# Kernel optimization log

Measured on AMD Instinct MI355X. Metric: run time of the kernel, lower is better.

Reference implementation:

```python
import jax, jax.numpy as jnp
import numpy as np

EPS = 1e-5

def layer_norm(x, g, b):
    m = x.mean(-1, keepdims=True)
    v = ((x - m) ** 2).mean(-1, keepdims=True)
    return (x - m) * jax.lax.rsqrt(v + EPS) * g + b

def setup_inputs() -> dict:
    key = jax.random.key(0)
    ks = jax.random.split(key, 8)
    H, T = 512, 256
    hidden_states = jax.random.normal(ks[0], (1, T, H), jnp.float32)
    U = jax.random.normal(ks[1], (H, H), jnp.float32) * 0.01
    W = jax.random.normal(ks[2], (H, H), jnp.float32) * 0.01
    a = jax.random.normal(ks[3], (H,), jnp.float32) * 0.01
    b = jax.random.normal(ks[4], (H,), jnp.float32) * 0.01
    gamma = jnp.ones((H,), jnp.float32)
    beta = jnp.zeros((H,), jnp.float32)
    targets = jax.random.randint(ks[5], (T,), 0, H)  # deterministic stand-in for torch.randint dummy targets
    return {"hidden_states": hidden_states, "U": U, "W": W, "a": a, "b": b,
            "gamma": gamma, "beta": beta, "targets": targets}

def reference(hidden_states, U, W, a, b, gamma, beta, targets):
    # batch must be 1 (torch.outer in the original requires 1-D vectors)
    h = hidden_states[0]                      # (T, H)
    z = jax.nn.relu(h @ U + a)                # (T, H) slow-path hidden

    # Per-timestep grads of CE(LayerNorm(z_t @ W + b), target_t) w.r.t. W, b
    def step_loss(z_t, tgt, W_, b_):
        y = layer_norm(z_t @ W_ + b_, gamma, beta)
        return -jax.nn.log_softmax(y)[tgt]
    grad_fn = jax.grad(step_loss, argnums=(2, 3))
    gradW, gradb = jax.vmap(grad_fn, in_axes=(0, 0, None, None))(z, targets, W, b)  # (T,H,H), (T,H)

    # W_update_t[p,q] = sum_{i<t} h_i[p] * h_t[q] * gradW_i[p,q]
    G = h[:, :, None] * gradW                 # (T, H, H)
    A = jnp.cumsum(G, axis=0) - G             # exclusive prefix sum over i
    W_upd = A * h[:, None, :]                 # (T, H, H)
    fastW = W - jnp.cumsum(W_upd, axis=0)     # cumulative fast weights per t

    # b_update_t[q] = h_t[q] * sum_{i<t} (sum_p h_i[p]) * gradb_i[q]
    c = h.sum(-1)                             # (T,)
    Bc = c[:, None] * gradb                   # (T, H)
    Bex = jnp.cumsum(Bc, axis=0) - Bc         # exclusive
    b_upd = h * Bex
    fastb = b - jnp.cumsum(b_upd, axis=0)     # (T, H)

    pre = jnp.einsum('th,thq->tq', z, fastW) + fastb
    out = layer_norm(pre, gamma, beta)        # (T, H)
    return out[None]                          # (1, T, H)
```

## Files before the change

### kernel.cpp

```cpp
#include <hip/hip_runtime.h>

#define T 256
#define H 512
#define EPSF 1e-5f

__device__ __forceinline__ float block_sum(float v, float* s4) {
    for (int o = 32; o; o >>= 1) v += __shfl_xor(v, o);
    int w = threadIdx.x >> 6;
    __syncthreads();
    if ((threadIdx.x & 63) == 0) s4[w] = v;
    __syncthreads();
    return s4[0] + s4[1] + s4[2] + s4[3];
}

__device__ __forceinline__ float block_max(float v, float* s4) {
    for (int o = 32; o; o >>= 1) v = fmaxf(v, __shfl_xor(v, o));
    int w = threadIdx.x >> 6;
    __syncthreads();
    if ((threadIdx.x & 63) == 0) s4[w] = v;
    __syncthreads();
    return fmaxf(fmaxf(s4[0], s4[1]), fmaxf(s4[2], s4[3]));
}

__global__ __launch_bounds__(256) void k1(
        const float* __restrict__ h, const float* __restrict__ U,
        const float* __restrict__ a, float* __restrict__ Z,
        float* __restrict__ HZ, float* __restrict__ c, float* __restrict__ S) {
    int bid = blockIdx.x, tid = threadIdx.x;
    int lane = tid & 63, w = tid >> 6;
    if (bid < 8) {
        __shared__ float csum[4][64];
        int q = bid * 64 + lane;
        int tbase = w * 64;
        float s = 0.f;
        for (int j = 0; j < 64; j += 8) {
            float v[8];
            #pragma unroll
            for (int u = 0; u < 8; ++u) v[u] = h[(tbase + j + u) * H + q];
            #pragma unroll
            for (int u = 0; u < 8; ++u) s += v[u];
        }
        csum[w][lane] = s;
        __syncthreads();
        float acc = 0.f;
        #pragma unroll
        for (int w2 = 0; w2 < 3; ++w2) if (w2 < w) acc += csum[w2][lane];
        for (int j = 0; j < 64; j += 8) {
            float v[8];
            #pragma unroll
            for (int u = 0; u < 8; ++u) v[u] = h[(tbase + j + u) * H + q];
            #pragma unroll
            for (int u = 0; u < 8; ++u) { acc += v[u]; S[(tbase + j + u) * H + q] = acc; }
        }
        return;
    }
    int b = bid - 8;
    int t0 = (b >> 2) * 2, qt = b & 3;
    __shared__ __align__(16) float sh[1024];
    __shared__ float2 part[3][2][64];
    __shared__ float s4[4];
    (void)s4;
    ((float4*)sh)[tid] = ((const float4*)(h + t0 * H))[tid];
    __syncthreads();

    if (qt == 0 && w < 2) {
        float s = 0.f;
        #pragma unroll
        for (int j = 0; j < 8; ++j) s += sh[w * 512 + lane + j * 64];
        for (int o = 32; o; o >>= 1) s += __shfl_xor(s, o);
        if (lane == 0) c[t0 + w] = s;
    }

    int qc = qt * 64 + lane;
    const float2* U2 = (const float2*)U;
    float2 acc0 = {0.f, 0.f}, acc1 = {0.f, 0.f};
    int kbeg = w * 128;
    for (int k0 = kbeg; k0 < kbeg + 128; k0 += 8) {
        float2 bv[8];
        #pragma unroll
        for (int u = 0; u < 8; ++u) bv[u] = U2[(k0 + u) * 256 + qc];
        float a0[8], a1[8];
        #pragma unroll
        for (int u = 0; u < 8; ++u) { a0[u] = sh[k0 + u]; a1[u] = sh[512 + k0 + u]; }
        #pragma unroll
        for (int u = 0; u < 8; ++u) {
            acc0.x += a0[u] * bv[u].x; acc0.y += a0[u] * bv[u].y;
            acc1.x += a1[u] * bv[u].x; acc1.y += a1[u] * bv[u].y;
        }
    }
    if (w) { part[w - 1][0][lane] = acc0; part[w - 1][1][lane] = acc1; }
    __syncthreads();
    if (w == 0) {
        #pragma unroll
        for (int p = 0; p < 3; ++p) {
            acc0.x += part[p][0][lane].x; acc0.y += part[p][0][lane].y;
            acc1.x += part[p][1][lane].x; acc1.y += part[p][1][lane].y;
        }
        float2 av = ((const float2*)a)[qc];
        float z0x = fmaxf(acc0.x + av.x, 0.f), z0y = fmaxf(acc0.y + av.y, 0.f);
        float z1x = fmaxf(acc1.x + av.x, 0.f), z1y = fmaxf(acc1.y + av.y, 0.f);
        float2 h0 = ((float2*)sh)[qc], h1 = ((float2*)sh)[256 + qc];
        ((float2*)Z)[t0 * 256 + qc]        = make_float2(z0x, z0y);
        ((float2*)Z)[(t0 + 1) * 256 + qc]  = make_float2(z1x, z1y);
        ((float2*)HZ)[t0 * 256 + qc]       = make_float2(h0.x * z0x, h0.y * z0y);
        ((float2*)HZ)[(t0 + 1) * 256 + qc] = make_float2(h1.x * z1x, h1.y * z1y);
    }
}

__global__ __launch_bounds__(256) void k2(
        const float* __restrict__ Z, const float* __restrict__ W,
        const float* __restrict__ bb, const float* __restrict__ HZ,
        const float* __restrict__ c, float* __restrict__ u0,
        float* __restrict__ Beta) {
    __shared__ __align__(16) float smem[2 * 8 * 516 + 256];
    int bid = blockIdx.x, tid = threadIdx.x;
    int lane = tid & 63, w = tid >> 6;
    if (bid < 512) {
        float* sh = smem;
        float2* part = (float2*)(smem + 1024);
        int t0 = (bid >> 2) * 2, qt = bid & 3;
        ((float4*)sh)[tid] = ((const float4*)(Z + t0 * H))[tid];
        __syncthreads();
        int qc = qt * 64 + lane;
        const float2* W2 = (const float2*)W;
        float2 acc0 = {0.f, 0.f}, acc1 = {0.f, 0.f};
        int kbeg = w * 128;
        for (int k0 = kbeg; k0 < kbeg + 128; k0 += 8) {
            float2 bv[8];
            #pragma unroll
            for (int u = 0; u < 8; ++u) bv[u] = W2[(k0 + u) * 256 + qc];
            float a0[8], a1[8];
            #pragma unroll
            for (int u = 0; u < 8; ++u) { a0[u] = sh[k0 + u]; a1[u] = sh[512 + k0 + u]; }
            #pragma unroll
            for (int u = 0; u < 8; ++u) {
                acc0.x += a0[u] * bv[u].x; acc0.y += a0[u] * bv[u].y;
                acc1.x += a1[u] * bv[u].x; acc1.y += a1[u] * bv[u].y;
            }
        }
        if (w) { part[((w - 1) * 2 + 0) * 64 + lane] = acc0; part[((w - 1) * 2 + 1) * 64 + lane] = acc1; }
        __syncthreads();
        if (w == 0) {
            #pragma unroll
            for (int p = 0; p < 3; ++p) {
                float2 p0 = part[(p * 2 + 0) * 64 + lane];
                float2 p1 = part[(p * 2 + 1) * 64 + lane];
                acc0.x += p0.x; acc0.y += p0.y;
                acc1.x += p1.x; acc1.y += p1.y;
            }
            float2 bv = ((const float2*)bb)[qc];
            ((float2*)u0)[t0 * 256 + qc]       = make_float2(acc0.x + bv.x, acc0.y + bv.y);
            ((float2*)u0)[(t0 + 1) * 256 + qc] = make_float2(acc1.x + bv.x, acc1.y + bv.y);
        }
    } else {
        int b = bid - 512;
        int ti = b >> 5, ii = b & 31;
        if (ii > ti) return;
        int t0 = ti * 8, i0 = ii * 8;
        float* Zs = smem;
        float* Hs = smem + 8 * 516;
        float* red = smem + 2 * 8 * 516;
        #pragma unroll
        for (int j = 0; j < 4; ++j) {
            int idx = tid + j * 256;
            int row = idx >> 7, col4 = idx & 127;
            float4 v = ((const float4*)(Z + (t0 + row) * H))[col4];
            *(float4*)&Zs[row * 516 + col4 * 4] = v;
            float4 g = ((const float4*)(HZ + (i0 + row) * H))[col4];
            *(float4*)&Hs[row * 516 + col4 * 4] = g;
        }
        __syncthreads();
        int ks = tid >> 6, r = (tid >> 3) & 7, ci = tid & 7;
        float acc = 0.f;
        int kb = ks * 128;
        #pragma unroll 4
        for (int k0 = kb; k0 < kb + 128; k0 += 8) {
            float4 z0 = *(float4*)&Zs[r * 516 + k0];
            float4 z1 = *(float4*)&Zs[r * 516 + k0 + 4];
            float4 h0 = *(float4*)&Hs[ci * 516 + k0];
            float4 h1 = *(float4*)&Hs[ci * 516 + k0 + 4];
            acc += z0.x * h0.x + z0.y * h0.y + z0.z * h0.z + z0.w * h0.w
                 + z1.x * h1.x + z1.y * h1.y + z1.z * h1.z + z1.w * h1.w;
        }
        red[ks * 64 + r * 8 + ci] = acc;
        __syncthreads();
        if (tid < 64) {
            int r2 = tid >> 3, c2 = tid & 7;
            float v = red[tid] + red[64 + tid] + red[128 + tid] + red[192 + tid];
            int t = t0 + r2, i = i0 + c2;
            Beta[t * 256 + i] = (i < t) ? v + c[i] : 0.f;
        }
    }
}

__global__ __launch_bounds__(256) void k3(
        const float* __restrict__ u0, const float* __restrict__ gamma,
        const float* __restrict__ beta, const int* __restrict__ targets,
        const float* __restrict__ S, float* __restrict__ D, float* __restrict__ SD) {
    __shared__ float s4[4];
    int t = blockIdx.x, tid = threadIdx.x;
    float2 uv = ((const float2*)u0)[t * 256 + tid];
    float2 gv = ((const float2*)gamma)[tid];
    float2 bv = ((const float2*)beta)[tid];

    float m = block_sum(uv.x + uv.y, s4) * (1.f / H);
    float d0 = uv.x - m, d1 = uv.y - m;
    float var = block_sum(d0 * d0 + d1 * d1, s4) * (1.f / H);
    float s = rsqrtf(var + EPSF);
    float xh0 = d0 * s, xh1 = d1 * s;
    float y0 = xh0 * gv.x + bv.x;
    float y1 = xh1 * gv.y + bv.y;

    float ymax = block_max(fmaxf(y0, y1), s4);
    float e0 = __expf(y0 - ymax), e1 = __expf(y1 - ymax);
    float Zs = block_sum(e0 + e1, s4);
    float invZ = 1.f / Zs;
    int tgt = targets[t];
    float g0 = e0 * invZ - (2 * tid == tgt ? 1.f : 0.f);
    float g1 = e1 * invZ - (2 * tid + 1 == tgt ? 1.f : 0.f);
    float gy0 = g0 * gv.x, gy1 = g1 * gv.y;

    float mgy = block_sum(gy0 + gy1, s4) * (1.f / H);
    float mgx = block_sum(gy0 * xh0 + gy1 * xh1, s4) * (1.f / H);

    float dd0 = s * (gy0 - mgy - xh0 * mgx);
    float dd1 = s * (gy1 - mgy - xh1 * mgx);
    float2 sv = ((const float2*)S)[t * 256 + tid];
    ((float2*)D)[t * 256 + tid]  = make_float2(dd0, dd1);
    ((float2*)SD)[t * 256 + tid] = make_float2(sv.x * dd0, sv.y * dd1);
}

__global__ __launch_bounds__(256) void k5(
        const float* __restrict__ Beta, const float* __restrict__ D,
        const float* __restrict__ SD, float* __restrict__ A1p,
        float* __restrict__ A2p) {
    int bid = blockIdx.x, tid = threadIdx.x;
    int t = bid >> 1, kh = bid & 1;
    int qc = tid;
    int ibeg = kh * 128;
    int kup;
    if (kh == 0) kup = (t >= 128) ? 128 : ((t + 7) & ~7);
    else         kup = (t > 128) ? ((t + 7) & ~7) : 128;
    const float2* D2 = (const float2*)D;
    const float2* SD2 = (const float2*)SD;
    float2 a1 = {0.f, 0.f}, a2 = {0.f, 0.f};
    for (int k0 = ibeg; k0 < kup; k0 += 8) {
        float2 dv[8], sv[8];
        #pragma unroll
        for (int u = 0; u < 8; ++u) {
            dv[u] = D2[(k0 + u) * 256 + qc];
            sv[u] = SD2[(k0 + u) * 256 + qc];
        }
        #pragma unroll
        for (int u = 0; u < 8; ++u) {
            float bw = Beta[t * 256 + k0 + u];
            a1.x += bw * dv[u].x; a1.y += bw * dv[u].y;
            a2.x += bw * sv[u].x; a2.y += bw * sv[u].y;
        }
    }
    ((float2*)A1p)[(kh * T + t) * 256 + qc] = a1;
    ((float2*)A2p)[(kh * T + t) * 256 + qc] = a2;
}

__global__ __launch_bounds__(256) void k6(
        const float* __restrict__ A1p, const float* __restrict__ A2p,
        const float* __restrict__ u0, const float* __restrict__ S,
        const float* __restrict__ gamma, const float* __restrict__ beta,
        float* __restrict__ out) {
    __shared__ float s4[4];
    int t = blockIdx.x, tid = threadIdx.x, qc = tid;
    float2 a1a = ((const float2*)A1p)[t * 256 + qc];
    float2 a1b = ((const float2*)A1p)[(T + t) * 256 + qc];
    float2 a2a = ((const float2*)A2p)[t * 256 + qc];
    float2 a2b = ((const float2*)A2p)[(T + t) * 256 + qc];
    float2 uv = ((const float2*)u0)[t * 256 + qc];
    float2 st = ((const float2*)S)[t * 256 + qc];
    float p0 = uv.x - st.x * (a1a.x + a1b.x) + (a2a.x + a2b.x);
    float p1 = uv.y - st.y * (a1a.y + a1b.y) + (a2a.y + a2b.y);
    float m = block_sum(p0 + p1, s4) * (1.f / H);
    float d0 = p0 - m, d1 = p1 - m;
    float var = block_sum(d0 * d0 + d1 * d1, s4) * (1.f / H);
    float s = rsqrtf(var + EPSF);
    float2 gv = ((const float2*)gamma)[qc];
    float2 bv = ((const float2*)beta)[qc];
    ((float2*)out)[t * 256 + qc] = make_float2(
        d0 * s * gv.x + bv.x, d1 * s * gv.y + bv.y);
}

extern "C" void kernel_launch(void* const* d_in, const int* in_sizes, int n_in,
                              void* d_out, int out_size, void* d_ws, size_t ws_size,
                              hipStream_t stream) {
    const float* h     = (const float*)d_in[0];
    const float* U     = (const float*)d_in[1];
    const float* W     = (const float*)d_in[2];
    const float* a     = (const float*)d_in[3];
    const float* b     = (const float*)d_in[4];
    const float* gamma = (const float*)d_in[5];
    const float* beta  = (const float*)d_in[6];
    const int*   tgt   = (const int*)d_in[7];
    float* out = (float*)d_out;

    float* ws = (float*)d_ws;
    float* Z    = ws;
    float* HZ   = Z    + T * H;
    float* u0   = HZ   + T * H;
    float* D    = u0   + T * H;
    float* SD   = D    + T * H;
    float* S    = SD   + T * H;
    float* A1p  = S    + T * H;
    float* A2p  = A1p  + 2 * T * H;
    float* c    = A2p  + 2 * T * H;
    float* Beta = c    + T;

    k1<<<520,  256, 0, stream>>>(h, U, a, Z, HZ, c, S);
    k2<<<1536, 256, 0, stream>>>(Z, W, b, HZ, c, u0, Beta);
    k3<<<T,    256, 0, stream>>>(u0, gamma, beta, tgt, S, D, SD);
    k5<<<2 * T, 256, 0, stream>>>(Beta, D, SD, A1p, A2p);
    k6<<<T,    256, 0, stream>>>(A1p, A2p, u0, S, gamma, beta, out);
}
```

Baseline: 114.4 us.

## Widen GEMM row tiles, compact triangular grid, fuse prefix-sum and final LayerNorm kernels

The k1 and k2 GEMM blocks now each process 8 timesteps instead of 2. This reuses every U/W load across 8 rows and cuts the block count. The triangular Beta part of k2 now launches only the lower-triangle tiles, using a sqrt-based index decode, instead of launching a full grid and returning early. k5 and k6 are merged into one kernel that handles 4 timesteps per block and does the full k-range reduction plus the final LayerNorm, which removes the A1p/A2p intermediate buffers and one launch. The trade-off is far fewer blocks (136, 64), so the GPU may be underused, plus more register pressure.

```diff
diff --git a/kernel.cpp b/kernel.cpp
--- a/kernel.cpp
+++ b/kernel.cpp
@@ -55,55 +55,65 @@
         return;
     }
     int b = bid - 8;
-    int t0 = (b >> 2) * 2, qt = b & 3;
-    __shared__ __align__(16) float sh[1024];
-    __shared__ float2 part[3][2][64];
-    __shared__ float s4[4];
-    (void)s4;
-    ((float4*)sh)[tid] = ((const float4*)(h + t0 * H))[tid];
-    __syncthreads();
-
-    if (qt == 0 && w < 2) {
-        float s = 0.f;
-        #pragma unroll
-        for (int j = 0; j < 8; ++j) s += sh[w * 512 + lane + j * 64];
-        for (int o = 32; o; o >>= 1) s += __shfl_xor(s, o);
-        if (lane == 0) c[t0 + w] = s;
+    int t0 = (b >> 2) * 8, qt = b & 3;
+    __shared__ __align__(16) float sh[8 * 512];
+    __shared__ float2 part[3][8][64];
+    #pragma unroll
+    for (int j = 0; j < 4; ++j)
+        ((float4*)sh)[tid + j * 256] = ((const float4*)(h + t0 * H))[tid + j * 256];
+    __syncthreads();
+
+    if (qt == 0) {
+        #pragma unroll
+        for (int rr = 0; rr < 2; ++rr) {
+            int r = w * 2 + rr;
+            float s = 0.f;
+            #pragma unroll
+            for (int j = 0; j < 8; ++j) s += sh[r * 512 + lane + j * 64];
+            for (int o = 32; o; o >>= 1) s += __shfl_xor(s, o);
+            if (lane == 0) c[t0 + r] = s;
+        }
     }
 
     int qc = qt * 64 + lane;
     const float2* U2 = (const float2*)U;
-    float2 acc0 = {0.f, 0.f}, acc1 = {0.f, 0.f};
+    float2 acc[8];
+    #pragma unroll
+    for (int r = 0; r < 8; ++r) acc[r] = make_float2(0.f, 0.f);
     int kbeg = w * 128;
     for (int k0 = kbeg; k0 < kbeg + 128; k0 += 8) {
         float2 bv[8];
         #pragma unroll
         for (int u = 0; u < 8; ++u) bv[u] = U2[(k0 + u) * 256 + qc];
-        float a0[8], a1[8];
-        #pragma unroll
-        for (int u = 0; u < 8; ++u) { a0[u] = sh[k0 + u]; a1[u] = sh[512 + k0 + u]; }
-        #pragma unroll
-        for (int u = 0; u < 8; ++u) {
-            acc0.x += a0[u] * bv[u].x; acc0.y += a0[u] * bv[u].y;
-            acc1.x += a1[u] * bv[u].x; acc1.y += a1[u] * bv[u].y;
-        }
-    }
-    if (w) { part[w - 1][0][lane] = acc0; part[w - 1][1][lane] = acc1; }
+        #pragma unroll
+        for (int r = 0; r < 8; ++r) {
+            float4 f0 = *(const float4*)&sh[r * 512 + k0];
+            float4 f1 = *(const float4*)&sh[r * 512 + k0 + 4];
+            float av[8] = {f0.x, f0.y, f0.z, f0.w, f1.x, f1.y, f1.z, f1.w};
+            #pragma unroll
+            for (int u = 0; u < 8; ++u) {
+                acc[r].x += av[u] * bv[u].x;
+                acc[r].y += av[u] * bv[u].y;
+            }
+        }
+    }
+    if (w) {
+        #pragma unroll
+        for (int r = 0; r < 8; ++r) part[w - 1][r][lane] = acc[r];
+    }
     __syncthreads();
     if (w == 0) {
-        #pragma unroll
-        for (int p = 0; p < 3; ++p) {
-            acc0.x += part[p][0][lane].x; acc0.y += part[p][0][lane].y;
-            acc1.x += part[p][1][lane].x; acc1.y += part[p][1][lane].y;
-        }
-        float2 av = ((const float2*)a)[qc];
-        float z0x = fmaxf(acc0.x + av.x, 0.f), z0y = fmaxf(acc0.y + av.y, 0.f);
-        float z1x = fmaxf(acc1.x + av.x, 0.f), z1y = fmaxf(acc1.y + av.y, 0.f);
-        float2 h0 = ((float2*)sh)[qc], h1 = ((float2*)sh)[256 + qc];
-        ((float2*)Z)[t0 * 256 + qc]        = make_float2(z0x, z0y);
-        ((float2*)Z)[(t0 + 1) * 256 + qc]  = make_float2(z1x, z1y);
-        ((float2*)HZ)[t0 * 256 + qc]       = make_float2(h0.x * z0x, h0.y * z0y);
-        ((float2*)HZ)[(t0 + 1) * 256 + qc] = make_float2(h1.x * z1x, h1.y * z1y);
+        float2 av2 = ((const float2*)a)[qc];
+        #pragma unroll
+        for (int r = 0; r < 8; ++r) {
+            float2 s0 = acc[r];
+            #pragma unroll
+            for (int p = 0; p < 3; ++p) { s0.x += part[p][r][lane].x; s0.y += part[p][r][lane].y; }
+            float zx = fmaxf(s0.x + av2.x, 0.f), zy = fmaxf(s0.y + av2.y, 0.f);
+            float hx = sh[r * 512 + 2 * qc], hy = sh[r * 512 + 2 * qc + 1];
+            ((float2*)Z)[(t0 + r) * 256 + qc]  = make_float2(zx, zy);
+            ((float2*)HZ)[(t0 + r) * 256 + qc] = make_float2(hx * zx, hy * zy);
+        }
     }
 }
 
@@ -112,50 +122,63 @@
         const float* __restrict__ bb, const float* __restrict__ HZ,
         const float* __restrict__ c, float* __restrict__ u0,
         float* __restrict__ Beta) {
-    __shared__ __align__(16) float smem[2 * 8 * 516 + 256];
+    __shared__ __align__(16) float smem[8512];
     int bid = blockIdx.x, tid = threadIdx.x;
     int lane = tid & 63, w = tid >> 6;
-    if (bid < 512) {
+    if (bid < 128) {
         float* sh = smem;
-        float2* part = (float2*)(smem + 1024);
-        int t0 = (bid >> 2) * 2, qt = bid & 3;
-        ((float4*)sh)[tid] = ((const float4*)(Z + t0 * H))[tid];
+        float2* part = (float2*)(smem + 4096);
+        int t0 = (bid >> 2) * 8, qt = bid & 3;
+        #pragma unroll
+        for (int j = 0; j < 4; ++j)
+            ((float4*)sh)[tid + j * 256] = ((const float4*)(Z + t0 * H))[tid + j * 256];
         __syncthreads();
         int qc = qt * 64 + lane;
         const float2* W2 = (const float2*)W;
-        float2 acc0 = {0.f, 0.f}, acc1 = {0.f, 0.f};
+        float2 acc[8];
+        #pragma unroll
+        for (int r = 0; r < 8; ++r) acc[r] = make_float2(0.f, 0.f);
         int kbeg = w * 128;
         for (int k0 = kbeg; k0 < kbeg + 128; k0 += 8) {
             float2 bv[8];
             #pragma unroll
             for (int u = 0; u < 8; ++u) bv[u] = W2[(k0 + u) * 256 + qc];
-            float a0[8], a1[8];
-            #pragma unroll
-            for (int u = 0; u < 8; ++u) { a0[u] = sh[k0 + u]; a1[u] = sh[512 + k0 + u]; }
-            #pragma unroll
-            for (int u = 0; u < 8; ++u) {
-                acc0.x += a0[u] * bv[u].x; acc0.y += a0[u] * bv[u].y;
-                acc1.x += a1[u] * bv[u].x; acc1.y += a1[u] * bv[u].y;
+            #pragma unroll
+            for (int r = 0; r < 8; ++r) {
+                float4 f0 = *(const float4*)&sh[r * 512 + k0];
+                float4 f1 = *(const float4*)&sh[r * 512 + k0 + 4];
+                float av[8] = {f0.x, f0.y, f0.z, f0.w, f1.x, f1.y, f1.z, f1.w};
+                #pragma unroll
+                for (int u = 0; u < 8; ++u) {
+                    acc[r].x += av[u] * bv[u].x;
+                    acc[r].y += av[u] * bv[u].y;
+                }
             }
         }
-        if (w) { part[((w - 1) * 2 + 0) * 64 + lane] = acc0; part[((w - 1) * 2 + 1) * 64 + lane] = acc1; }
+        if (w) {
+            #pragma unroll
+            for (int r = 0; r < 8; ++r) part[((w - 1) * 8 + r) * 64 + lane] = acc[r];
+        }
         __syncthreads();
         if (w == 0) {
-            #pragma unroll
-            for (int p = 0; p < 3; ++p) {
-                float2 p0 = part[(p * 2 + 0) * 64 + lane];
-                float2 p1 = part[(p * 2 + 1) * 64 + lane];
-                acc0.x += p0.x; acc0.y += p0.y;
-                acc1.x += p1.x; acc1.y += p1.y;
+            float2 bv2 = ((const float2*)bb)[qc];
+            #pragma unroll
+            for (int r = 0; r < 8; ++r) {
+                float2 s0 = acc[r];
+                #pragma unroll
+                for (int p = 0; p < 3; ++p) {
+                    float2 pv = part[(p * 8 + r) * 64 + lane];
+                    s0.x += pv.x; s0.y += pv.y;
+                }
+                ((float2*)u0)[(t0 + r) * 256 + qc] = make_float2(s0.x + bv2.x, s0.y + bv2.y);
             }
-            float2 bv = ((const float2*)bb)[qc];
-            ((float2*)u0)[t0 * 256 + qc]       = make_float2(acc0.x + bv.x, acc0.y + bv.y);
-            ((float2*)u0)[(t0 + 1) * 256 + qc] = make_float2(acc1.x + bv.x, acc1.y + bv.y);
         }
     } else {
-        int b = bid - 512;
-        int ti = b >> 5, ii = b & 31;
-        if (ii > ti) return;
+        int b = bid - 128;
+        int ti = (int)((sqrtf(8.f * (float)b + 1.f) - 1.f) * 0.5f);
+        while ((ti + 1) * (ti + 2) / 2 <= b) ++ti;
+        while (ti * (ti + 1) / 2 > b) --ti;
+        int ii = b - ti * (ti + 1) / 2;
         int t0 = ti * 8, i0 = ii * 8;
         float* Zs = smem;
         float* Hs = smem + 8 * 516;
@@ -230,21 +253,24 @@
     ((float2*)SD)[t * 256 + tid] = make_float2(sv.x * dd0, sv.y * dd1);
 }
 
-__global__ __launch_bounds__(256) void k5(
+__global__ __launch_bounds__(256) void k4(
         const float* __restrict__ Beta, const float* __restrict__ D,
-        const float* __restrict__ SD, float* __restrict__ A1p,
-        float* __restrict__ A2p) {
-    int bid = blockIdx.x, tid = threadIdx.x;
-    int t = bid >> 1, kh = bid & 1;
+        const float* __restrict__ SD, const float* __restrict__ u0,
+        const float* __restrict__ S, const float* __restrict__ gamma,
+        const float* __restrict__ beta, float* __restrict__ out) {
+    __shared__ __align__(16) float Brow[4 * 256];
+    __shared__ float s4[4];
+    int t0 = blockIdx.x * 4, tid = threadIdx.x;
+    ((float4*)Brow)[tid] = ((const float4*)(Beta + t0 * 256))[tid];
+    __syncthreads();
     int qc = tid;
-    int ibeg = kh * 128;
-    int kup;
-    if (kh == 0) kup = (t >= 128) ? 128 : ((t + 7) & ~7);
-    else         kup = (t > 128) ? ((t + 7) & ~7) : 128;
     const float2* D2 = (const float2*)D;
     const float2* SD2 = (const float2*)SD;
-    float2 a1 = {0.f, 0.f}, a2 = {0.f, 0.f};
-    for (int k0 = ibeg; k0 < kup; k0 += 8) {
+    float2 a1[4], a2[4];
+    #pragma unroll
+    for (int r = 0; r < 4; ++r) { a1[r] = make_float2(0.f, 0.f); a2[r] = make_float2(0.f, 0.f); }
+    int kup = (t0 + 10) & ~7;
+    for (int k0 = 0; k0 < kup; k0 += 8) {
         float2 dv[8], sv[8];
         #pragma unroll
         for (int u = 0; u < 8; ++u) {
@@ -253,38 +279,30 @@
         }
         #pragma unroll
         for (int u = 0; u < 8; ++u) {
-            float bw = Beta[t * 256 + k0 + u];
-            a1.x += bw * dv[u].x; a1.y += bw * dv[u].y;
-            a2.x += bw * sv[u].x; a2.y += bw * sv[u].y;
-        }
-    }
-    ((float2*)A1p)[(kh * T + t) * 256 + qc] = a1;
-    ((float2*)A2p)[(kh * T + t) * 256 + qc] = a2;
-}
-
-__global__ __launch_bounds__(256) void k6(
-        const float* __restrict__ A1p, const float* __restrict__ A2p,
-        const float* __restrict__ u0, const float* __restrict__ S,
-        const float* __restrict__ gamma, const float* __restrict__ beta,
-        float* __restrict__ out) {
-    __shared__ float s4[4];
-    int t = blockIdx.x, tid = threadIdx.x, qc = tid;
-    float2 a1a = ((const float2*)A1p)[t * 256 + qc];
-    float2 a1b = ((const float2*)A1p)[(T + t) * 256 + qc];
-    float2 a2a = ((const float2*)A2p)[t * 256 + qc];
-    float2 a2b = ((const float2*)A2p)[(T + t) * 256 + qc];
-    float2 uv = ((const float2*)u0)[t * 256 + qc];
-    float2 st = ((const float2*)S)[t * 256 + qc];
-    float p0 = uv.x - st.x * (a1a.x + a1b.x) + (a2a.x + a2b.x);
-    float p1 = uv.y - st.y * (a1a.y + a1b.y) + (a2a.y + a2b.y);
-    float m = block_sum(p0 + p1, s4) * (1.f / H);
-    float d0 = p0 - m, d1 = p1 - m;
-    float var = block_sum(d0 * d0 + d1 * d1, s4) * (1.f / H);
-    float s = rsqrtf(var + EPSF);
+            #pragma unroll
+            for (int r = 0; r < 4; ++r) {
+                float bw = Brow[r * 256 + k0 + u];
+                a1[r].x += bw * dv[u].x; a1[r].y += bw * dv[u].y;
+                a2[r].x += bw * sv[u].x; a2[r].y += bw * sv[u].y;
+            }
+        }
+    }
     float2 gv = ((const float2*)gamma)[qc];
     float2 bv = ((const float2*)beta)[qc];
-    ((float2*)out)[t * 256 + qc] = make_float2(
-        d0 * s * gv.x + bv.x, d1 * s * gv.y + bv.y);
+    #pragma unroll
+    for (int r = 0; r < 4; ++r) {
+        int t = t0 + r;
+        float2 uv = ((const float2*)u0)[t * 256 + qc];
+        float2 st = ((const float2*)S)[t * 256 + qc];
+        float p0 = uv.x - st.x * a1[r].x + a2[r].x;
+        float p1 = uv.y - st.y * a1[r].y + a2[r].y;
+        float m = block_sum(p0 + p1, s4) * (1.f / H);
+        float d0 = p0 - m, d1 = p1 - m;
+        float var = block_sum(d0 * d0 + d1 * d1, s4) * (1.f / H);
+        float s = rsqrtf(var + EPSF);
+        ((float2*)out)[t * 256 + qc] = make_float2(
+            d0 * s * gv.x + bv.x, d1 * s * gv.y + bv.y);
+    }
 }
 
 extern "C" void kernel_launch(void* const* d_in, const int* in_sizes, int n_in,
@@ -307,14 +325,11 @@
     float* D    = u0   + T * H;
     float* SD   = D    + T * H;
     float* S    = SD   + T * H;
-    float* A1p  = S    + T * H;
-    float* A2p  = A1p  + 2 * T * H;
-    float* c    = A2p  + 2 * T * H;
+    float* c    = S    + T * H;
     float* Beta = c    + T;
 
-    k1<<<520,  256, 0, stream>>>(h, U, a, Z, HZ, c, S);
-    k2<<<1536, 256, 0, stream>>>(Z, W, b, HZ, c, u0, Beta);
-    k3<<<T,    256, 0, stream>>>(u0, gamma, beta, tgt, S, D, SD);
-    k5<<<2 * T, 256, 0, stream>>>(Beta, D, SD, A1p, A2p);
-    k6<<<T,    256, 0, stream>>>(A1p, A2p, u0, S, gamma, beta, out);
-}
+    k1<<<136, 256, 0, stream>>>(h, U, a, Z, HZ, c, S);
+    k2<<<656, 256, 0, stream>>>(Z, W, b, HZ, c, u0, Beta);
+    k3<<<T,   256, 0, stream>>>(u0, gamma, beta, tgt, S, D, SD);
+    k4<<<64,  256, 0, stream>>>(Beta, D, SD, u0, S, gamma, beta, out);
+}
```

After: 133.4 us. 16.7% more time.
